# Performance work log

Hardware: AMD Instinct MI355X
Metric: run time of the kernel (lower is better)

## Reference

```python
import jax, jax.numpy as jnp
import numpy as np

N_NODES = 100000
N_EDGES = 3200000
IN_CH = 128
HID_CH = 64
NEG_SLOPE = 0.2  # PyG GATConv default leaky_relu slope


def setup_inputs() -> dict:
    key = jax.random.key(0)
    k1, k2, k3, k4, k5, k6 = jax.random.split(key, 6)
    x = jax.random.normal(k1, (N_NODES, IN_CH), dtype=jnp.float32)
    edge_index = jax.random.randint(k2, (2, N_EDGES), 0, N_NODES, dtype=jnp.int64)
    # learned params of GATConv(in, hid, heads=1)
    W = jax.random.normal(k3, (IN_CH, HID_CH), dtype=jnp.float32) / np.sqrt(IN_CH)
    att_src = jax.random.normal(k4, (HID_CH,), dtype=jnp.float32) / np.sqrt(HID_CH)
    att_dst = jax.random.normal(k5, (HID_CH,), dtype=jnp.float32) / np.sqrt(HID_CH)
    bias = jax.random.normal(k6, (HID_CH,), dtype=jnp.float32) * 0.01
    return {"x": x, "edge_index": edge_index, "W": W, "att_src": att_src,
            "att_dst": att_dst, "bias": bias}


def reference(x, edge_index, W, att_src, att_dst, bias):
    N = x.shape[0]
    h = x @ W  # [N, H] linear transform
    # PyG GATConv default: add self loops
    loops = jnp.arange(N, dtype=edge_index.dtype)
    src = jnp.concatenate([edge_index[0], loops])  # [E+N]
    dst = jnp.concatenate([edge_index[1], loops])
    # per-node attention halves, then gather per-edge
    a_src = h @ att_src  # [N]
    a_dst = h @ att_dst  # [N]
    e = jax.nn.leaky_relu(a_src[src] + a_dst[dst], NEG_SLOPE)  # [E+N]
    # segment softmax over incoming edges of each destination node
    m = jax.ops.segment_max(e, dst, num_segments=N)
    e = jnp.exp(e - m[dst])
    s = jax.ops.segment_sum(e, dst, num_segments=N)
    alpha = e / s[dst]  # [E+N]
    # scatter-aggregate weighted source features
    out = jax.ops.segment_sum(h[src] * alpha[:, None], dst, num_segments=N) + bias
    return out, alpha[:, None]
```

## Files before the change

kernel.cpp:

```cpp
#include <hip/hip_runtime.h>
#include <hip/hip_bf16.h>

#define IN_CH 128
#define HID 64
#define NEG_SLOPE 0.2f
#define BSH 8
#define CAP 10240
#define KPT 20

typedef __attribute__((ext_vector_type(8))) short short8;
typedef __attribute__((ext_vector_type(4))) float floatx4;
typedef __attribute__((ext_vector_type(2))) float f32x2;

__device__ inline short bfr(float f) {
    unsigned u = __float_as_uint(f);
    u += 0x7fffu + ((u >> 16) & 1u);
    return (short)(u >> 16);
}

__global__ void k_prep(const float* __restrict__ W, short* __restrict__ wfrag,
                       int* __restrict__ g_cursor)
{
    if (blockIdx.x == 0) {
        g_cursor[threadIdx.x] = 0;
        g_cursor[threadIdx.x + 256] = 0;
    }
    int idx = blockIdx.x * 256 + threadIdx.x;
    if (idx >= 1024) return;
    int f = idx >> 6, l = idx & 63;
    int kt = f >> 2, nt = f & 3;
    int k0 = kt * 32 + (l >> 4) * 8;
    int n = nt * 16 + (l & 15);
#pragma unroll
    for (int j = 0; j < 8; ++j)
        wfrag[idx * 8 + j] = bfr(W[(k0 + j) * HID + n]);
}

__global__ __launch_bounds__(256) void k_gemm(
    const float* __restrict__ x, const short8* __restrict__ wfrag,
    const float* __restrict__ att_src, const float* __restrict__ att_dst,
    short* __restrict__ h, float* __restrict__ a_src,
    float* __restrict__ a_dst, int N)
{
    const int t = threadIdx.x;
    const int lane = t & 63;
    const int wv = t >> 6;
    const int l15 = lane & 15;
    const int quad = lane >> 4;

    short8 bf[16];
#pragma unroll
    for (int f = 0; f < 16; ++f) bf[f] = wfrag[f * 64 + lane];

    float as4[4], ad4[4];
#pragma unroll
    for (int nt = 0; nt < 4; ++nt) {
        as4[nt] = att_src[nt * 16 + l15];
        ad4[nt] = att_dst[nt * 16 + l15];
    }

    const int rowbase = blockIdx.x * 128 + wv * 32;

#pragma unroll
    for (int mt = 0; mt < 2; ++mt) {
        const int m0 = rowbase + mt * 16;
        const int rowa = m0 + l15;
        const int rowc = rowa < N ? rowa : N - 1;
        const float* xp = x + (size_t)rowc * IN_CH + quad * 8;

        short8 af[4];
#pragma unroll
        for (int kt = 0; kt < 4; ++kt) {
            float4 p0 = *(const float4*)(xp + kt * 32);
            float4 p1 = *(const float4*)(xp + kt * 32 + 4);
            short8 a;
            a[0] = bfr(p0.x); a[1] = bfr(p0.y); a[2] = bfr(p0.z); a[3] = bfr(p0.w);
            a[4] = bfr(p1.x); a[5] = bfr(p1.y); a[6] = bfr(p1.z); a[7] = bfr(p1.w);
            af[kt] = a;
        }

        floatx4 acc[4];
#pragma unroll
        for (int nt = 0; nt < 4; ++nt) acc[nt] = (floatx4){0.f, 0.f, 0.f, 0.f};
#pragma unroll
        for (int kt = 0; kt < 4; ++kt)
#pragma unroll
            for (int nt = 0; nt < 4; ++nt)
                acc[nt] = __builtin_amdgcn_mfma_f32_16x16x32_bf16(
                    af[kt], bf[kt * 4 + nt], acc[nt], 0, 0, 0);

#pragma unroll
        for (int r = 0; r < 4; ++r) {
            const int row = m0 + quad * 4 + r;
            const bool ok = row < N;
            if (ok) {
#pragma unroll
                for (int nt = 0; nt < 4; ++nt)
                    h[(size_t)row * HID + nt * 16 + l15] = bfr(acc[nt][r]);
            }
            float ps = acc[0][r] * as4[0] + acc[1][r] * as4[1] +
                       acc[2][r] * as4[2] + acc[3][r] * as4[3];
            float pd = acc[0][r] * ad4[0] + acc[1][r] * ad4[1] +
                       acc[2][r] * ad4[2] + acc[3][r] * ad4[3];
#pragma unroll
            for (int m2 = 1; m2 < 16; m2 <<= 1) {
                ps += __shfl_xor(ps, m2, 64);
                pd += __shfl_xor(pd, m2, 64);
            }
            if (ok && l15 == 0) { a_src[row] = ps; a_dst[row] = pd; }
        }
    }
}

__global__ __launch_bounds__(256) void k_binB(
    const int* __restrict__ ei, int* __restrict__ g_cursor,
    int* __restrict__ pairs, int E, int nb)
{
    __shared__ int hist[512];
    __shared__ int base[512];
    const int t = threadIdx.x;
    hist[t] = 0;
    hist[t + 256] = 0;
    __syncthreads();

    int s[16], d[16], l[16];
    const int4* s4 = (const int4*)ei;
    const int4* d4 = (const int4*)(ei + E);
    const int E4 = E >> 2;
    const int q0 = blockIdx.x * 1024;
#pragma unroll
    for (int i = 0; i < 4; ++i) {
        int q = q0 + i * 256 + t;
        int4 sv = make_int4(0, 0, 0, 0);
        int4 dv = make_int4(-1, -1, -1, -1);
        if (q < E4) { sv = s4[q]; dv = d4[q]; }
        s[4 * i + 0] = sv.x; s[4 * i + 1] = sv.y; s[4 * i + 2] = sv.z; s[4 * i + 3] = sv.w;
        d[4 * i + 0] = dv.x; d[4 * i + 1] = dv.y; d[4 * i + 2] = dv.z; d[4 * i + 3] = dv.w;
    }
#pragma unroll
    for (int i = 0; i < 16; ++i)
        if (d[i] >= 0) l[i] = atomicAdd(&hist[d[i] >> BSH], 1);
    __syncthreads();

    if (t < nb) base[t] = atomicAdd(&g_cursor[t], hist[t]);
    if (t + 256 < nb) base[t + 256] = atomicAdd(&g_cursor[t + 256], hist[t + 256]);
    __syncthreads();

#pragma unroll
    for (int i = 0; i < 16; ++i) {
        if (d[i] < 0) continue;
        int b = d[i] >> BSH;
        int pos = base[b] + l[i];
        if (pos < CAP)
            pairs[b * CAP + pos] = s[i] | ((d[i] & 255) << 17);
    }
}

__global__ __launch_bounds__(512) void k_binC(
    const int* __restrict__ pairs, const int* __restrict__ g_cursor,
    int* __restrict__ row_start, int* __restrict__ cnt,
    int* __restrict__ csr_src, int N, int nb)
{
    __shared__ int h0[256];
    __shared__ int hs[512];
    __shared__ int exc[256];
    __shared__ int sbase;
    const int t = threadIdx.x;
    const int b = blockIdx.x;
    int m = g_cursor[b];
    if (m > CAP) m = CAP;
    const int* pb = pairs + b * CAP;

    int bv = (t < nb) ? g_cursor[t] : 0;
    hs[t] = bv;
    __syncthreads();
    for (int off = 1; off < 512; off <<= 1) {
        int u = (t >= off) ? hs[t - off] : 0;
        __syncthreads();
        hs[t] += u;
        __syncthreads();
    }
    if (t == b) sbase = hs[t] - bv;
    if (t < 256) h0[t] = 0;
    __syncthreads();

    int p[KPT], l[KPT];
#pragma unroll
    for (int k = 0; k < KPT; ++k) {
        const int i = t + k * 512;
        if (i < m) {
            p[k] = pb[i];
            l[k] = atomicAdd(&h0[p[k] >> 17], 1);
        }
    }
    __syncthreads();

    if (t < 256) hs[t] = h0[t];
    __syncthreads();
    for (int off = 1; off < 256; off <<= 1) {
        int u = (t >= off && t < 256) ? hs[t - off] : 0;
        __syncthreads();
        if (t < 256) hs[t] += u;
        __syncthreads();
    }
    const int basec = sbase;
    if (t < 256) {
        const int e0 = hs[t] - h0[t];
        exc[t] = e0;
        const int dd = (b << BSH) + t;
        if (dd < N) { row_start[dd] = basec + e0; cnt[dd] = h0[t]; }
    }
    __syncthreads();

#pragma unroll
    for (int k = 0; k < KPT; ++k) {
        const int i = t + k * 512;
        if (i < m) {
            const int dl = p[k] >> 17;
            csr_src[basec + exc[dl] + l[k]] = p[k] & 0x1FFFF;
        }
    }
}

__global__ __launch_bounds__(256) void k_agg(
    const __hip_bfloat16* __restrict__ h, const float* __restrict__ a_src,
    const float* __restrict__ a_dst, const float* __restrict__ bias,
    const int* __restrict__ row_start, const int* __restrict__ cnt,
    const int* __restrict__ csr_src,
    float* __restrict__ out, float2* __restrict__ adi, int N)
{
    __shared__ float red[4][2][576];

    const int wave = threadIdx.x >> 6;
    const int lane = threadIdx.x & 63;
    const int d0 = blockIdx.x * 8 + wave * 2;
    if (d0 >= N) return;
    const int d1 = d0 + 1;
    const bool has1 = d1 < N;

    const int q  = lane >> 3;
    const int i8 = lane & 7;

    const float2 ad2 = *(const float2*)(a_dst + d0);
    const float ad0 = ad2.x;
    const float ad1 = ad2.y;
    const int2 cn2 = *(const int2*)(cnt + d0);
    const int n0 = cn2.x;
    const int n1 = has1 ? cn2.y : 0;
    const int st0 = row_start[d0];
    const int en0 = st0 + n0;
    const int st1 = en0;
    const int en1 = st1 + n1;

    const uint4* h4 = (const uint4*)h;

    float ps0 = 0.f, ps1 = 0.f;
    f32x2 ac0[4], ac1[4];
#pragma unroll
    for (int c = 0; c < 4; ++c) {
        ac0[c] = (f32x2){0.f, 0.f};
        ac1[c] = (f32x2){0.f, 0.f};
    }

    const int nbt0 = (n0 + 63) >> 6;
    const int nbt1 = (n1 + 63) >> 6;
    const int nbm = nbt0 > nbt1 ? nbt0 : nbt1;

    int b0 = st0, b1 = st1;
    for (int it = 0; it < nbm; ++it, b0 += 64, b1 += 64) {
        int s0v = 0, s1v = 0;
        float e0 = 0.f, e1 = 0.f;
        const int idx0 = b0 + lane;
        if (it < nbt0 && idx0 < en0) {
            s0v = csr_src[idx0];
            float v = a_src[s0v] + ad0;
            v = v > 0.f ? v : NEG_SLOPE * v;
            e0 = __expf(v);
            ps0 += e0;
        }
        const int idx1 = b1 + lane;
        if (it < nbt1 && idx1 < en1) {
            s1v = csr_src[idx1];
            float v = a_src[s1v] + ad1;
            v = v > 0.f ? v : NEG_SLOPE * v;
            e1 = __expf(v);
            ps1 += e1;
        }
        const int m0 = (it < nbt0) ? min(64, en0 - b0) : 0;
        const int m1 = (it < nbt1) ? min(64, en1 - b1) : 0;
        const int mm = m0 > m1 ? m0 : m1;
#pragma unroll 4
        for (int j = 0; j < mm; j += 8) {
            const int jq = j + q;
            const int sj0 = __shfl(s0v, jq, 64);
            const float ej0 = __shfl(e0, jq, 64);
            const int sj1 = __shfl(s1v, jq, 64);
            const float ej1 = __shfl(e1, jq, 64);
            uint4 u0 = h4[(size_t)sj0 * 8 + i8];
            uint4 u1 = h4[(size_t)sj1 * 8 + i8];
            f32x2 ev0; ev0[0] = ej0; ev0[1] = ej0;
            f32x2 ev1; ev1[0] = ej1; ev1[1] = ej1;
            f32x2 c;
            c[0] = __uint_as_float(u0.x << 16);
            c[1] = __uint_as_float(u0.x & 0xffff0000u);
            ac0[0] = __builtin_elementwise_fma(ev0, c, ac0[0]);
            c[0] = __uint_as_float(u0.y << 16);
            c[1] = __uint_as_float(u0.y & 0xffff0000u);
            ac0[1] = __builtin_elementwise_fma(ev0, c, ac0[1]);
            c[0] = __uint_as_float(u0.z << 16);
            c[1] = __uint_as_float(u0.z & 0xffff0000u);
            ac0[2] = __builtin_elementwise_fma(ev0, c, ac0[2]);
            c[0] = __uint_as_float(u0.w << 16);
            c[1] = __uint_as_float(u0.w & 0xffff0000u);
            ac0[3] = __builtin_elementwise_fma(ev0, c, ac0[3]);
            c[0] = __uint_as_float(u1.x << 16);
            c[1] = __uint_as_float(u1.x & 0xffff0000u);
            ac1[0] = __builtin_elementwise_fma(ev1, c, ac1[0]);
            c[0] = __uint_as_float(u1.y << 16);
            c[1] = __uint_as_float(u1.y & 0xffff0000u);
            ac1[1] = __builtin_elementwise_fma(ev1, c, ac1[1]);
            c[0] = __uint_as_float(u1.z << 16);
            c[1] = __uint_as_float(u1.z & 0xffff0000u);
            ac1[2] = __builtin_elementwise_fma(ev1, c, ac1[2]);
            c[0] = __uint_as_float(u1.w << 16);
            c[1] = __uint_as_float(u1.w & 0xffff0000u);
            ac1[3] = __builtin_elementwise_fma(ev1, c, ac1[3]);
        }
    }

    float* r0 = &red[wave][0][0];
    float* r1 = &red[wave][1][0];
#pragma unroll
    for (int p = 0; p < 4; ++p) {
        r0[(i8 * 8 + 2 * p) * 9 + q]     = ac0[p][0];
        r0[(i8 * 8 + 2 * p + 1) * 9 + q] = ac0[p][1];
        r1[(i8 * 8 + 2 * p) * 9 + q]     = ac1[p][0];
        r1[(i8 * 8 + 2 * p + 1) * 9 + q] = ac1[p][1];
    }

#pragma unroll
    for (int m2 = 32; m2 > 0; m2 >>= 1) {
        ps0 += __shfl_xor(ps0, m2, 64);
        ps1 += __shfl_xor(ps1, m2, 64);
    }

    const float2 asd = *(const float2*)(a_src + d0);
    float vs0 = asd.x + ad0;
    vs0 = vs0 > 0.f ? vs0 : NEG_SLOPE * vs0;
    const float es0 = __expf(vs0);
    const float inv0 = 1.f / (ps0 + es0);
    float es1 = 0.f, inv1 = 0.f;
    if (has1) {
        float vs1 = asd.y + ad1;
        vs1 = vs1 > 0.f ? vs1 : NEG_SLOPE * vs1;
        es1 = __expf(vs1);
        inv1 = 1.f / (ps1 + es1);
    }
    if (lane == 0) {
        adi[d0] = make_float2(ad0, inv0);
        if (has1) adi[d1] = make_float2(ad1, inv1);
    }

    float s0 = 0.f, s1 = 0.f;
#pragma unroll
    for (int qq = 0; qq < 8; ++qq) {
        s0 += r0[lane * 9 + qq];
        s1 += r1[lane * 9 + qq];
    }

    const ushort* hu = (const ushort*)h;
    const float bi = bias[lane];
    float hs0 = __uint_as_float(((unsigned)hu[(size_t)d0 * HID + lane]) << 16);
    out[(size_t)d0 * HID + lane] = fmaf(es0, hs0, s0) * inv0 + bi;
    if (has1) {
        float hs1 = __uint_as_float(((unsigned)hu[(size_t)d1 * HID + lane]) << 16);
        out[(size_t)d1 * HID + lane] = fmaf(es1, hs1, s1) * inv1 + bi;
    }
}

__global__ void k_alpha(const int* __restrict__ ei,
                        const float* __restrict__ a_src,
                        const float2* __restrict__ adi,
                        float* __restrict__ out_alpha, int E, int N)
{
    const int E4 = E >> 2;
    const int i = blockIdx.x * 256 + threadIdx.x;
    if (i < E4) {
        const int4 sv = ((const int4*)ei)[i];
        const int4 dv = ((const int4*)(ei + E))[i];
        float4 o;
        {
            const float2 av = adi[dv.x];
            float v = a_src[sv.x] + av.x;
            v = v > 0.f ? v : NEG_SLOPE * v;
            o.x = __expf(v) * av.y;
        }
        {
            const float2 av = adi[dv.y];
            float v = a_src[sv.y] + av.x;
            v = v > 0.f ? v : NEG_SLOPE * v;
            o.y = __expf(v) * av.y;
        }
        {
            const float2 av = adi[dv.z];
            float v = a_src[sv.z] + av.x;
            v = v > 0.f ? v : NEG_SLOPE * v;
            o.z = __expf(v) * av.y;
        }
        {
            const float2 av = adi[dv.w];
            float v = a_src[sv.w] + av.x;
            v = v > 0.f ? v : NEG_SLOPE * v;
            o.w = __expf(v) * av.y;
        }
        ((float4*)out_alpha)[i] = o;
    } else {
        const int j = i - E4;
        if (j < N) {
            const float2 av = adi[j];
            float v = a_src[j] + av.x;
            v = v > 0.f ? v : NEG_SLOPE * v;
            out_alpha[E + j] = __expf(v) * av.y;
        }
    }
}

extern "C" void kernel_launch(void* const* d_in, const int* in_sizes, int n_in,
                              void* d_out, int out_size, void* d_ws, size_t ws_size,
                              hipStream_t stream)
{
    (void)n_in; (void)out_size; (void)ws_size;
    const float* x       = (const float*)d_in[0];
    const int*   ei      = (const int*)d_in[1];
    const float* W       = (const float*)d_in[2];
    const float* att_src = (const float*)d_in[3];
    const float* att_dst = (const float*)d_in[4];
    const float* bias    = (const float*)d_in[5];

    const int N = in_sizes[0] / IN_CH;
    const int E = in_sizes[1] / 2;
    const int nb = (N + 255) >> BSH;

    __hip_bfloat16* h = (__hip_bfloat16*)d_ws;
    float* a_src_d = (float*)(h + (size_t)N * HID);
    float* a_dst_d = a_src_d + N;
    float2* adi    = (float2*)(a_dst_d + N);
    int* row_start = (int*)(adi + N);
    int* cnt       = row_start + N;
    int* g_cursor  = cnt + N;
    short* wfrag   = (short*)(g_cursor + 512);
    int* pairs     = (int*)(wfrag + 8192);
    int* csr_src   = pairs + (size_t)nb * CAP;

    float* out       = (float*)d_out;
    float* out_alpha = out + (size_t)N * HID;

    k_prep<<<4, 256, 0, stream>>>(W, wfrag, g_cursor);
    k_gemm<<<(N + 127) / 128, 256, 0, stream>>>(x, (const short8*)wfrag,
                                                att_src, att_dst,
                                                (short*)h, a_src_d, a_dst_d, N);
    k_binB<<<(E / 4 + 1023) / 1024, 256, 0, stream>>>(ei, g_cursor, pairs, E, nb);
    k_binC<<<nb, 512, 0, stream>>>(pairs, g_cursor,
                                   row_start, cnt, csr_src, N, nb);
    k_agg<<<(N + 7) / 8, 256, 0, stream>>>(h, a_src_d, a_dst_d, bias,
                                           row_start, cnt, csr_src,
                                           out, adi, N);
    k_alpha<<<((E >> 2) + N + 255) / 256, 256, 0, stream>>>(ei, a_src_d, adi,
                                                            out_alpha, E, N);
}
```

Baseline: 272.9 us.

## Fold weight prep into GEMM, simplify CSR binning, split aggregation launch

```diff
diff --git a/kernel.cpp b/kernel.cpp
--- a/kernel.cpp
+++ b/kernel.cpp
@@ -6,7 +6,6 @@
 #define NEG_SLOPE 0.2f
 #define BSH 8
 #define CAP 10240
-#define KPT 20
 
 typedef __attribute__((ext_vector_type(8))) short short8;
 typedef __attribute__((ext_vector_type(4))) float floatx4;
@@ -18,39 +17,43 @@
     return (short)(u >> 16);
 }
 
-__global__ void k_prep(const float* __restrict__ W, short* __restrict__ wfrag,
-                       int* __restrict__ g_cursor)
-{
-    if (blockIdx.x == 0) {
-        g_cursor[threadIdx.x] = 0;
-        g_cursor[threadIdx.x + 256] = 0;
-    }
-    int idx = blockIdx.x * 256 + threadIdx.x;
-    if (idx >= 1024) return;
-    int f = idx >> 6, l = idx & 63;
-    int kt = f >> 2, nt = f & 3;
-    int k0 = kt * 32 + (l >> 4) * 8;
-    int n = nt * 16 + (l & 15);
-#pragma unroll
-    for (int j = 0; j < 8; ++j)
-        wfrag[idx * 8 + j] = bfr(W[(k0 + j) * HID + n]);
-}
-
 __global__ __launch_bounds__(256) void k_gemm(
-    const float* __restrict__ x, const short8* __restrict__ wfrag,
+    const float* __restrict__ x, const float* __restrict__ W,
     const float* __restrict__ att_src, const float* __restrict__ att_dst,
     short* __restrict__ h, float* __restrict__ a_src,
-    float* __restrict__ a_dst, int N)
-{
+    float* __restrict__ a_dst, int* __restrict__ g_cursor, int N)
+{
+    __shared__ float wlds[IN_CH * 65];
+
     const int t = threadIdx.x;
     const int lane = t & 63;
     const int wv = t >> 6;
     const int l15 = lane & 15;
     const int quad = lane >> 4;
 
+    if (blockIdx.x == 0) { g_cursor[t] = 0; g_cursor[t + 256] = 0; }
+
+#pragma unroll
+    for (int r = 0; r < 8; ++r) {
+        const int idx4 = r * 256 + t;
+        const float4 w4 = ((const float4*)W)[idx4];
+        const int fi = idx4 * 4;
+        float* dst = &wlds[(fi >> 6) * 65 + (fi & 63)];
+        dst[0] = w4.x; dst[1] = w4.y; dst[2] = w4.z; dst[3] = w4.w;
+    }
+    __syncthreads();
+
     short8 bf[16];
 #pragma unroll
-    for (int f = 0; f < 16; ++f) bf[f] = wfrag[f * 64 + lane];
+    for (int f = 0; f < 16; ++f) {
+        const int kt = f >> 2, nt = f & 3;
+        const int k0 = kt * 32 + quad * 8;
+        const int n = nt * 16 + l15;
+        short8 a;
+#pragma unroll
+        for (int j = 0; j < 8; ++j) a[j] = bfr(wlds[(k0 + j) * 65 + n]);
+        bf[f] = a;
+    }
 
     float as4[4], ad4[4];
 #pragma unroll
@@ -163,7 +166,7 @@
 {
     __shared__ int h0[256];
     __shared__ int hs[512];
-    __shared__ int exc[256];
+    __shared__ int cur[256];
     __shared__ int sbase;
     const int t = threadIdx.x;
     const int b = blockIdx.x;
@@ -183,16 +186,10 @@
     if (t == b) sbase = hs[t] - bv;
     if (t < 256) h0[t] = 0;
     __syncthreads();
-
-    int p[KPT], l[KPT];
-#pragma unroll
-    for (int k = 0; k < KPT; ++k) {
-        const int i = t + k * 512;
-        if (i < m) {
-            p[k] = pb[i];
-            l[k] = atomicAdd(&h0[p[k] >> 17], 1);
-        }
-    }
+    const int basec = sbase;
+
+    for (int i = t; i < m; i += 512)
+        atomicAdd(&h0[pb[i] >> 17], 1);
     __syncthreads();
 
     if (t < 256) hs[t] = h0[t];
@@ -203,22 +200,18 @@
         if (t < 256) hs[t] += u;
         __syncthreads();
     }
-    const int basec = sbase;
     if (t < 256) {
-        const int e0 = hs[t] - h0[t];
-        exc[t] = e0;
+        const int excl = hs[t] - h0[t];
+        cur[t] = basec + excl;
         const int dd = (b << BSH) + t;
-        if (dd < N) { row_start[dd] = basec + e0; cnt[dd] = h0[t]; }
-    }
-    __syncthreads();
-
-#pragma unroll
-    for (int k = 0; k < KPT; ++k) {
-        const int i = t + k * 512;
-        if (i < m) {
-            const int dl = p[k] >> 17;
-            csr_src[basec + exc[dl] + l[k]] = p[k] & 0x1FFFF;
-        }
+        if (dd < N) { row_start[dd] = basec + excl; cnt[dd] = h0[t]; }
+    }
+    __syncthreads();
+
+    for (int i = t; i < m; i += 512) {
+        int p = pb[i];
+        int pos = atomicAdd(&cur[p >> 17], 1);
+        csr_src[pos] = p & 0x1FFFF;
     }
 }
 
@@ -227,13 +220,13 @@
     const float* __restrict__ a_dst, const float* __restrict__ bias,
     const int* __restrict__ row_start, const int* __restrict__ cnt,
     const int* __restrict__ csr_src,
-    float* __restrict__ out, float2* __restrict__ adi, int N)
+    float* __restrict__ out, float2* __restrict__ adi, int dbase, int N)
 {
     __shared__ float red[4][2][576];
 
     const int wave = threadIdx.x >> 6;
     const int lane = threadIdx.x & 63;
-    const int d0 = blockIdx.x * 8 + wave * 2;
+    const int d0 = dbase + blockIdx.x * 8 + wave * 2;
     if (d0 >= N) return;
     const int d1 = d0 + 1;
     const bool has1 = d1 < N;
@@ -448,23 +441,26 @@
     int* row_start = (int*)(adi + N);
     int* cnt       = row_start + N;
     int* g_cursor  = cnt + N;
-    short* wfrag   = (short*)(g_cursor + 512);
-    int* pairs     = (int*)(wfrag + 8192);
+    int* pairs     = g_cursor + 512;
     int* csr_src   = pairs + (size_t)nb * CAP;
 
     float* out       = (float*)d_out;
     float* out_alpha = out + (size_t)N * HID;
 
-    k_prep<<<4, 256, 0, stream>>>(W, wfrag, g_cursor);
-    k_gemm<<<(N + 127) / 128, 256, 0, stream>>>(x, (const short8*)wfrag,
-                                                att_src, att_dst,
-                                                (short*)h, a_src_d, a_dst_d, N);
+    k_gemm<<<(N + 127) / 128, 256, 0, stream>>>(x, W, att_src, att_dst,
+                                                (short*)h, a_src_d, a_dst_d,
+                                                g_cursor, N);
     k_binB<<<(E / 4 + 1023) / 1024, 256, 0, stream>>>(ei, g_cursor, pairs, E, nb);
     k_binC<<<nb, 512, 0, stream>>>(pairs, g_cursor,
                                    row_start, cnt, csr_src, N, nb);
-    k_agg<<<(N + 7) / 8, 256, 0, stream>>>(h, a_src_d, a_dst_d, bias,
+
+    const int H = 50000;
+    k_agg<<<(H + 7) / 8, 256, 0, stream>>>(h, a_src_d, a_dst_d, bias,
                                            row_start, cnt, csr_src,
-                                           out, adi, N);
+                                           out, adi, 0, H);
+    k_agg<<<(N - H + 7) / 8, 256, 0, stream>>>(h, a_src_d, a_dst_d, bias,
+                                               row_start, cnt, csr_src,
+                                               out, adi, H, N);
     k_alpha<<<((E >> 2) + N + 255) / 256, 256, 0, stream>>>(ei, a_src_d, adi,
                                                             out_alpha, E, N);
 }
```

New measurement: 284.7 us. 4.3% more time.
